# Performance work log

Hardware: AMD Instinct MI355X
Metric: run time of the kernel (lower is better)

## Reference

```python
import jax, jax.numpy as jnp
from jax import lax
import numpy as np

RATIO = 0.25
RADIUS = 0.2


def _fps(xyz, npoint):
    # iterative farthest point sampling, sequential over npoint via lax.scan
    B, N, _ = xyz.shape
    far0 = jax.random.randint(jax.random.key(42), (B,), 0, N)
    dist0 = jnp.full((B, N), 1e10, xyz.dtype)

    def step(carry, _):
        distance, far = carry
        centroid = jnp.take_along_axis(xyz, far[:, None, None], axis=1)  # (B,1,3)
        d = jnp.sum((xyz - centroid) ** 2, axis=-1)                      # (B,N)
        distance = jnp.minimum(distance, d)
        return (distance, jnp.argmax(distance, axis=-1)), far

    _, idxs = lax.scan(step, (dist0, far0), None, length=npoint)  # (npoint,B)
    return jnp.transpose(idxs)  # (B,npoint)


def _gather(pts, idx):
    # pts (B,N,C), idx (B,...) int -> (B,...,C)
    return jax.vmap(lambda p, i: p[i])(pts, idx)


def reference(xyz, points, w1, b1, w2, b2, w3, b3):
    B, N, _ = xyz.shape
    S = int(N * RATIO)
    fps_idx = _fps(xyz, S)                 # (B,S)
    new_xyz = _gather(xyz, fps_idx)        # (B,S,3)

    # ball query with nsample = N (module passes xyz.shape[1])
    sqr = (jnp.sum(new_xyz ** 2, -1)[:, :, None]
           + jnp.sum(xyz ** 2, -1)[:, None, :]
           - 2.0 * jnp.einsum('bsc,bnc->bsn', new_xyz, xyz))  # (B,S,N)
    gidx = jnp.where(sqr > RADIUS ** 2, N, jnp.arange(N)[None, None, :])
    gidx = jnp.sort(gidx, axis=-1)         # (B,S,N), sentinel N sorts last
    first = gidx[:, :, 0:1]
    idx = jnp.where(gidx == N, first, gidx)  # (B,S,N)

    grouped_xyz = _gather(xyz, idx) - new_xyz[:, :, None, :]       # (B,S,N,3)
    grouped_pts = _gather(jnp.transpose(points, (0, 2, 1)), idx)   # (B,S,N,C)
    x = jnp.concatenate([grouped_xyz, grouped_pts], axis=-1)       # (B,S,N,3+C)

    # 1x1 convs == pointwise channel linears, ReLU except last
    x = jax.nn.relu(jnp.einsum('bsnc,oc->bsno', x, w1) + b1)
    x = jax.nn.relu(jnp.einsum('bsnc,oc->bsno', x, w2) + b2)
    x = jnp.einsum('bsnc,oc->bsno', x, w3) + b3

    new_points = jnp.transpose(jnp.max(x, axis=2), (0, 2, 1))  # (B,C',S)
    return new_xyz, new_points


def setup_inputs() -> dict:
    key = jax.random.key(0)
    ks = jax.random.split(key, 8)
    return {
        'xyz': jax.random.uniform(ks[0], (2, 2048, 3), dtype=jnp.float32),
        'points': jax.random.normal(ks[1], (2, 13, 2048), dtype=jnp.float32),
        'w1': 0.1 * jax.random.normal(ks[2], (32, 16), dtype=jnp.float32),
        'b1': 0.1 * jax.random.normal(ks[3], (32,), dtype=jnp.float32),
        'w2': 0.1 * jax.random.normal(ks[4], (32, 32), dtype=jnp.float32),
        'b2': 0.1 * jax.random.normal(ks[5], (32,), dtype=jnp.float32),
        'w3': 0.1 * jax.random.normal(ks[6], (64, 32), dtype=jnp.float32),
        'b3': 0.1 * jax.random.normal(ks[7], (64,), dtype=jnp.float32),
    }
```

## Files before the change

kernel.cpp:

```cpp
#include <hip/hip_runtime.h>
#include <stdint.h>

#define NPTS 2048
#define SOUT 512
#define NB   2
#define TB   256
#define PPT  8
#define NW   4
#define FMAGIC 0xC0DE0000u

typedef float vf2 __attribute__((ext_vector_type(2)));

__device__ __forceinline__ float wave_allmax_f32(float v) {
    int x = __float_as_int(v); int t;
    t = __builtin_amdgcn_update_dpp(x, x, 0x111, 0xF, 0xF, true); v = fmaxf(v, __int_as_float(t)); x = __float_as_int(v);
    t = __builtin_amdgcn_update_dpp(x, x, 0x112, 0xF, 0xF, true); v = fmaxf(v, __int_as_float(t)); x = __float_as_int(v);
    t = __builtin_amdgcn_update_dpp(x, x, 0x114, 0xF, 0xF, true); v = fmaxf(v, __int_as_float(t)); x = __float_as_int(v);
    t = __builtin_amdgcn_update_dpp(x, x, 0x118, 0xF, 0xF, true); v = fmaxf(v, __int_as_float(t)); x = __float_as_int(v);
    t = __builtin_amdgcn_update_dpp(x, x, 0x142, 0xA, 0xF, true); v = fmaxf(v, __int_as_float(t)); x = __float_as_int(v);
    t = __builtin_amdgcn_update_dpp(x, x, 0x143, 0xC, 0xF, true); v = fmaxf(v, __int_as_float(t)); x = __float_as_int(v);
    return __int_as_float(__builtin_amdgcn_readlane(x, 63));
}
__device__ __forceinline__ float lane_bcast(float v, int l) {
    return __int_as_float(__builtin_amdgcn_readlane(__float_as_int(v), l));
}
__device__ __forceinline__ float4 sel4(bool c, float4 A, float4 B) {
    float4 r;
    r.x = c ? A.x : B.x; r.y = c ? A.y : B.y;
    r.z = c ? A.z : B.z; r.w = c ? A.w : B.w;
    return r;
}

template<bool FUSED>
__device__ __forceinline__ void fps_role(const float* __restrict__ xb,
                                         float* __restrict__ ob,
                                         unsigned* flagp, int far,
                                         float4* slot , float* scf,
                                         int t) {
    const int lane = t & 63;
    const int wvl  = t >> 6;
    float v24[24];
    {
        const float4* src = (const float4*)(xb + t * PPT * 3);
#pragma unroll
        for (int j = 0; j < 6; ++j) {
            float4 a = src[j];
            v24[j*4+0] = a.x; v24[j*4+1] = a.y; v24[j*4+2] = a.z; v24[j*4+3] = a.w;
        }
    }
    vf2 PX[4], PY[4], PZ[4], DD[4];
#pragma unroll
    for (int j = 0; j < 4; ++j) {
        PX[j].x = v24[(2*j)*3+0]; PX[j].y = v24[(2*j+1)*3+0];
        PY[j].x = v24[(2*j)*3+1]; PY[j].y = v24[(2*j+1)*3+1];
        PZ[j].x = v24[(2*j)*3+2]; PZ[j].y = v24[(2*j+1)*3+2];
        DD[j].x = 1e10f; DD[j].y = 1e10f;
    }
    float cx = xb[far*3+0], cy = xb[far*3+1], cz = xb[far*3+2];

    for (int s = 0; s < SOUT - 1; ++s) {
        if (FUSED) {
            if (wvl == 3) {
                if (lane == 32 && s >= 16 && (s & 15) == 0)
                    __hip_atomic_store(flagp, FMAGIC + (unsigned)s,
                                       __ATOMIC_RELEASE, __HIP_MEMORY_SCOPE_AGENT);
                if (lane >= 32 && lane < 35) {
                    float v = (lane == 32) ? cx : ((lane == 33) ? cy : cz);
                    unsigned* o = (unsigned*)ob + s * 3 + (lane - 32);
                    __hip_atomic_store(o, __float_as_uint(v),
                                       __ATOMIC_RELAXED, __HIP_MEMORY_SCOPE_AGENT);
                }
            }
        } else {
            if (t == 0) { scf[s*3+0] = cx; scf[s*3+1] = cy; scf[s*3+2] = cz; }
        }
        {
#pragma clang fp contract(off)
            vf2 vcx; vcx.x = cx; vcx.y = cx;
            vf2 vcy; vcy.x = cy; vcy.y = cy;
            vf2 vcz; vcz.x = cz; vcz.y = cz;
#pragma unroll
            for (int j = 0; j < 4; ++j) {
                vf2 dx = PX[j] - vcx;
                vf2 dy = PY[j] - vcy;
                vf2 dz = PZ[j] - vcz;
                vf2 d2 = (dx*dx + dy*dy) + dz*dz;
                DD[j].x = fminf(DD[j].x, d2.x);
                DD[j].y = fminf(DD[j].y, d2.y);
            }
        }
        float v1[4], x1v[4], y1v[4], z1v[4];
#pragma unroll
        for (int j = 0; j < 4; ++j) {
            bool l = DD[j].x >= DD[j].y;
            v1[j]  = l ? DD[j].x : DD[j].y;
            x1v[j] = l ? PX[j].x : PX[j].y;
            y1v[j] = l ? PY[j].x : PY[j].y;
            z1v[j] = l ? PZ[j].x : PZ[j].y;
        }
        float v2v[2], x2v[2], y2v[2], z2v[2];
#pragma unroll
        for (int j = 0; j < 2; ++j) {
            bool l = v1[2*j] >= v1[2*j+1];
            v2v[j] = l ? v1[2*j]  : v1[2*j+1];
            x2v[j] = l ? x1v[2*j] : x1v[2*j+1];
            y2v[j] = l ? y1v[2*j] : y1v[2*j+1];
            z2v[j] = l ? z1v[2*j] : z1v[2*j+1];
        }
        bool lf = v2v[0] >= v2v[1];
        float bv = lf ? v2v[0] : v2v[1];
        float bx = lf ? x2v[0] : x2v[1];
        float by = lf ? y2v[0] : y2v[1];
        float bz = lf ? z2v[0] : z2v[1];
        float wmax = wave_allmax_f32(bv);
        unsigned long long msk = __ballot(bv == wmax);
        int l0 = (int)__builtin_ctzll(msk);
        float wx = lane_bcast(bx, l0);
        float wy = lane_bcast(by, l0);
        float wz = lane_bcast(bz, l0);
        const int par = s & 1;
        if (lane == 0) slot[par*NW + wvl] = make_float4(wmax, wx, wy, wz);
        if (FUSED) {
            __builtin_amdgcn_s_waitcnt(0xC07F);
            __builtin_amdgcn_s_barrier();
        } else {
            __syncthreads();
        }
        float4 a0 = slot[par*NW + 0];
        float4 a1 = slot[par*NW + 1];
        float4 a2 = slot[par*NW + 2];
        float4 a3 = slot[par*NW + 3];
        float4 m01 = sel4(a1.x > a0.x, a1, a0);
        float4 m23 = sel4(a3.x > a2.x, a3, a2);
        float4 mf  = sel4(m23.x > m01.x, m23, m01);
        cx = mf.y; cy = mf.z; cz = mf.w;
    }
    if (FUSED) {
        if (wvl == 3) {
            if (lane >= 32 && lane < 35) {
                float v = (lane == 32) ? cx : ((lane == 33) ? cy : cz);
                unsigned* o = (unsigned*)ob + (SOUT - 1) * 3 + (lane - 32);
                __hip_atomic_store(o, __float_as_uint(v),
                                   __ATOMIC_RELAXED, __HIP_MEMORY_SCOPE_AGENT);
            }
            if (lane == 32)
                __hip_atomic_store(flagp, FMAGIC + 512u,
                                   __ATOMIC_RELEASE, __HIP_MEMORY_SCOPE_AGENT);
        }
    } else {
        if (t == 0) {
            scf[(SOUT-1)*3+0] = cx; scf[(SOUT-1)*3+1] = cy; scf[(SOUT-1)*3+2] = cz;
        }
        __syncthreads();
        for (int i = t; i < SOUT * 3; i += TB) ob[i] = scf[i];
    }
}

__device__ __forceinline__ void group_role(
        const float* __restrict__ xyz,  const float* __restrict__ points,
        const float* __restrict__ w1,   const float* __restrict__ b1,
        const float* __restrict__ w2,   const float* __restrict__ b2,
        const float* __restrict__ w3,   const float* __restrict__ b3,
        const float* __restrict__ new_xyz, float* __restrict__ new_points,
        const unsigned* flags, unsigned short* sidx, float* sh2,
        int lane, int q) {
    float wf3[32];
    {
        const float4* w3v = (const float4*)(w3 + lane * 32);
#pragma unroll
        for (int j = 0; j < 8; ++j) {
            float4 v = w3v[j];
            wf3[j*4+0] = v.x; wf3[j*4+1] = v.y; wf3[j*4+2] = v.z; wf3[j*4+3] = v.w;
        }
    }
    const float rb3 = b3[lane];
    const int b = q >> 9;
    const int s = q & (SOUT - 1);

    if (flags) {
        const unsigned* flagp = flags + (b << 6);
        if (lane == 0) {
            const unsigned tgt = FMAGIC + (unsigned)s + 1u;
            int polls = 0;
            for (;;) {
                unsigned v = __hip_atomic_load(flagp, __ATOMIC_ACQUIRE,
                                               __HIP_MEMORY_SCOPE_AGENT);
                if (v >= tgt && v <= FMAGIC + 512u) break;
                if (++polls > (1 << 18)) break;
                __builtin_amdgcn_s_sleep(32);
            }
        }
        __threadfence();
    }
    const unsigned* nx = (const unsigned*)new_xyz + (size_t)q * 3;
    const float qx = __uint_as_float(__hip_atomic_load(nx + 0, __ATOMIC_RELAXED, __HIP_MEMORY_SCOPE_AGENT));
    const float qy = __uint_as_float(__hip_atomic_load(nx + 1, __ATOMIC_RELAXED, __HIP_MEMORY_SCOPE_AGENT));
    const float qz = __uint_as_float(__hip_atomic_load(nx + 2, __ATOMIC_RELAXED, __HIP_MEMORY_SCOPE_AGENT));
    const float qs = __fadd_rn(__fadd_rn(__fmul_rn(qx,qx), __fmul_rn(qy,qy)), __fmul_rn(qz,qz));
    const float* xb = xyz    + (size_t)b * NPTS * 3;
    const float* pb = points + (size_t)b * 13 * NPTS;

    int cnt = 0;
    const unsigned long long lm = (1ull << lane) - 1ull;
    for (int r = 0; r < NPTS / 64; ++r) {
        int n = r * 64 + lane;
        float x = xb[n*3+0], y = xb[n*3+1], z = xb[n*3+2];
        float pn = __fadd_rn(__fadd_rn(__fmul_rn(x,x), __fmul_rn(y,y)), __fmul_rn(z,z));
        float dt = __fadd_rn(__fadd_rn(__fmul_rn(qx,x), __fmul_rn(qy,y)), __fmul_rn(qz,z));
        float sqr = __fsub_rn(__fadd_rn(qs, pn), __fmul_rn(2.0f, dt));
        bool sel = !(sqr > 0.04f);
        unsigned long long m = __ballot(sel);
        if (sel) sidx[cnt + __popcll(m & lm)] = (unsigned short)n;
        cnt += (int)__popcll(m);
    }
    const int K = cnt;
    const int nfirst = (int)sidx[0];

    float mx = -3.0e38f;
    for (int tb = 0; tb < K; tb += 64) {
        int m = tb + lane;
        int n = (m < K) ? (int)sidx[m] : nfirst;
        float f[16];
        f[0] = xb[n*3+0] - qx;
        f[1] = xb[n*3+1] - qy;
        f[2] = xb[n*3+2] - qz;
#pragma unroll
        for (int c = 0; c < 13; ++c) f[3+c] = pb[c*NPTS + n];
        float h1[32];
#pragma unroll
        for (int o = 0; o < 32; ++o) {
            float acc = b1[o];
            const float4* wr = (const float4*)(w1 + o*16);
#pragma unroll
            for (int c4 = 0; c4 < 4; ++c4) {
                float4 wv = wr[c4];
                acc = fmaf(f[c4*4+0], wv.x, acc);
                acc = fmaf(f[c4*4+1], wv.y, acc);
                acc = fmaf(f[c4*4+2], wv.z, acc);
                acc = fmaf(f[c4*4+3], wv.w, acc);
            }
            h1[o] = fmaxf(acc, 0.0f);
        }
        float h2[32];
#pragma unroll
        for (int o = 0; o < 32; ++o) {
            float acc = b2[o];
            const float4* wr = (const float4*)(w2 + o*32);
#pragma unroll
            for (int c4 = 0; c4 < 8; ++c4) {
                float4 wv = wr[c4];
                acc = fmaf(h1[c4*4+0], wv.x, acc);
                acc = fmaf(h1[c4*4+1], wv.y, acc);
                acc = fmaf(h1[c4*4+2], wv.z, acc);
                acc = fmaf(h1[c4*4+3], wv.w, acc);
            }
            h2[o] = fmaxf(acc, 0.0f);
        }
        {
            float4* row = (float4*)(sh2 + lane * 36);
#pragma unroll
            for (int c4 = 0; c4 < 8; ++c4)
                row[c4] = make_float4(h2[c4*4+0], h2[c4*4+1], h2[c4*4+2], h2[c4*4+3]);
        }
        int rows = K - tb; if (rows > 64) rows = 64;
#pragma unroll 4
        for (int n2 = 0; n2 < rows; ++n2) {
            const float4* hr = (const float4*)(sh2 + n2 * 36);
            float acc = rb3;
#pragma unroll
            for (int c4 = 0; c4 < 8; ++c4) {
                float4 h = hr[c4];
                acc = fmaf(h.x, wf3[c4*4+0], acc);
                acc = fmaf(h.y, wf3[c4*4+1], acc);
                acc = fmaf(h.z, wf3[c4*4+2], acc);
                acc = fmaf(h.w, wf3[c4*4+3], acc);
            }
            mx = fmaxf(mx, acc);
        }
    }
    new_points[((size_t)b * 64 + lane) * SOUT + s] = mx;
}

__global__ __launch_bounds__(TB, 1) void fused_kernel(
        const float* __restrict__ xyz,  const float* __restrict__ points,
        const float* __restrict__ w1,   const float* __restrict__ b1,
        const float* __restrict__ w2,   const float* __restrict__ b2,
        const float* __restrict__ w3,   const float* __restrict__ b3,
        float* __restrict__ new_xyz, float* __restrict__ new_points,
        unsigned* flags, int far0, int far1) {
    __shared__ float4 s_slot[2 * NW];
    __shared__ unsigned short s_sidx[4 * NPTS];
    __shared__ __align__(16) float s_sh2[4 * 64 * 36];
    const int blk = blockIdx.x;
    const int tid = threadIdx.x;
    if (blk < 2) {
        const int bg = blk;
        fps_role<true>(xyz + (size_t)bg * NPTS * 3,
                       new_xyz + (size_t)bg * SOUT * 3,
                       flags + (bg << 6),
                       (bg == 0) ? far0 : far1,
                       s_slot, nullptr, tid);
    } else {
        const int lane = tid & 63;
        const int wvl  = tid >> 6;
        const int q    = (blk - 2) * 4 + wvl;
        group_role(xyz, points, w1, b1, w2, b2, w3, b3, new_xyz, new_points,
                   flags, s_sidx + wvl * NPTS, s_sh2 + wvl * 64 * 36, lane, q);
    }
}

__global__ __launch_bounds__(TB, 1) void fps_kernel(const float* __restrict__ xyz,
                                                    float* __restrict__ new_xyz,
                                                    int far0, int far1) {
    __shared__ float4 s_slot[2 * NW];
    __shared__ __align__(16) float s_scf[SOUT * 3];
    const int bg = blockIdx.x;
    fps_role<false>(xyz + (size_t)bg * NPTS * 3, new_xyz + (size_t)bg * SOUT * 3,
                    nullptr, (bg == 0) ? far0 : far1, s_slot, s_scf, threadIdx.x);
}
__global__ __launch_bounds__(64, 1) void group_kernel(
        const float* __restrict__ xyz,  const float* __restrict__ points,
        const float* __restrict__ w1,   const float* __restrict__ b1,
        const float* __restrict__ w2,   const float* __restrict__ b2,
        const float* __restrict__ w3,   const float* __restrict__ b3,
        const float* __restrict__ new_xyz, float* __restrict__ new_points) {
    __shared__ unsigned short s_sidx[NPTS];
    __shared__ __align__(16) float s_sh2[64 * 36];
    group_role(xyz, points, w1, b1, w2, b2, w3, b3, new_xyz, new_points,
               nullptr, s_sidx, s_sh2, threadIdx.x, blockIdx.x);
}

static inline uint32_t rotl32(uint32_t x, int r) { return (x << r) | (x >> (32 - r)); }
static void threefry2x32_host(uint32_t k0, uint32_t k1, uint32_t& x0, uint32_t& x1) {
    const int R[2][4] = {{13,15,26,6},{17,29,16,24}};
    uint32_t ks[3] = {k0, k1, k0 ^ k1 ^ 0x1BD11BDAu};
    x0 += ks[0]; x1 += ks[1];
    for (int i = 0; i < 5; ++i) {
        for (int j = 0; j < 4; ++j) { x0 += x1; x1 = rotl32(x1, R[i & 1][j]); x1 ^= x0; }
        x0 += ks[(i + 1) % 3];
        x1 += ks[(i + 2) % 3] + (uint32_t)(i + 1);
    }
}

extern "C" void kernel_launch(void* const* d_in, const int* in_sizes, int n_in,
                              void* d_out, int out_size, void* d_ws, size_t ws_size,
                              hipStream_t stream) {
    const float* xyz    = (const float*)d_in[0];
    const float* points = (const float*)d_in[1];
    const float* w1 = (const float*)d_in[2];
    const float* b1 = (const float*)d_in[3];
    const float* w2 = (const float*)d_in[4];
    const float* b2 = (const float*)d_in[5];
    const float* w3 = (const float*)d_in[6];
    const float* b3 = (const float*)d_in[7];
    float* out        = (float*)d_out;
    float* new_xyz    = out;
    float* new_points = out + NB * SOUT * 3;

    uint32_t k2a = 0, k2b = 1; threefry2x32_host(0u, 42u, k2a, k2b);
    uint32_t u0 = 0, u1 = 0;  threefry2x32_host(k2a, k2b, u0, u1);
    uint32_t v0 = 0, v1 = 1;  threefry2x32_host(k2a, k2b, v0, v1);
    int far0 = (int)((u0 ^ u1) & (NPTS - 1));
    int far1 = (int)((v0 ^ v1) & (NPTS - 1));

    if (ws_size >= 512) {
        hipLaunchKernelGGL(fused_kernel, dim3(2 + NB * SOUT / 4), dim3(TB), 0, stream,
                           xyz, points, w1, b1, w2, b2, w3, b3,
                           new_xyz, new_points, (unsigned*)d_ws, far0, far1);
    } else {
        hipLaunchKernelGGL(fps_kernel, dim3(NB), dim3(TB), 0, stream,
                           xyz, new_xyz, far0, far1);
        hipLaunchKernelGGL(group_kernel, dim3(NB * SOUT), dim3(64), 0, stream,
                           xyz, points, w1, b1, w2, b2, w3, b3, new_xyz, new_points);
    }
}
```

Measured before the change: 360.9 us.

## Run farthest point sampling in a single wave to drop block barriers

The FPS role now runs on a single 64-lane wave. Each lane holds 32 points instead of 8, so the per-iteration LDS slot exchange and block barrier across four waves are gone; the wave reduction and lane broadcast alone pick the next centroid. This removes 511 serialized barriers from the sequential critical path. In exchange each wave does four times the distance work per step and uses more registers, and the other three waves of the FPS blocks sit idle.

```diff
diff --git a/kernel.cpp b/kernel.cpp
--- a/kernel.cpp
+++ b/kernel.cpp
@@ -5,8 +5,6 @@
 #define SOUT 512
 #define NB   2
 #define TB   256
-#define PPT  8
-#define NW   4
 #define FMAGIC 0xC0DE0000u
 
 typedef float vf2 __attribute__((ext_vector_type(2)));
@@ -24,135 +22,112 @@
 __device__ __forceinline__ float lane_bcast(float v, int l) {
     return __int_as_float(__builtin_amdgcn_readlane(__float_as_int(v), l));
 }
-__device__ __forceinline__ float4 sel4(bool c, float4 A, float4 B) {
-    float4 r;
-    r.x = c ? A.x : B.x; r.y = c ? A.y : B.y;
-    r.z = c ? A.z : B.z; r.w = c ? A.w : B.w;
-    return r;
-}
 
 template<bool FUSED>
-__device__ __forceinline__ void fps_role(const float* __restrict__ xb,
-                                         float* __restrict__ ob,
-                                         unsigned* flagp, int far,
-                                         float4* slot , float* scf,
-                                         int t) {
-    const int lane = t & 63;
-    const int wvl  = t >> 6;
-    float v24[24];
+__device__ __forceinline__ void fps_role_sw(const float* __restrict__ xb,
+                                            float* __restrict__ ob,
+                                            unsigned* flagp, int far, int lane) {
+    vf2 PX[16], PY[16], PZ[16], DD[16];
     {
-        const float4* src = (const float4*)(xb + t * PPT * 3);
-#pragma unroll
-        for (int j = 0; j < 6; ++j) {
-            float4 a = src[j];
-            v24[j*4+0] = a.x; v24[j*4+1] = a.y; v24[j*4+2] = a.z; v24[j*4+3] = a.w;
-        }
-    }
-    vf2 PX[4], PY[4], PZ[4], DD[4];
-#pragma unroll
-    for (int j = 0; j < 4; ++j) {
-        PX[j].x = v24[(2*j)*3+0]; PX[j].y = v24[(2*j+1)*3+0];
-        PY[j].x = v24[(2*j)*3+1]; PY[j].y = v24[(2*j+1)*3+1];
-        PZ[j].x = v24[(2*j)*3+2]; PZ[j].y = v24[(2*j+1)*3+2];
-        DD[j].x = 1e10f; DD[j].y = 1e10f;
+        const float4* src = (const float4*)(xb + (size_t)lane * 96);
+#pragma unroll
+        for (int g = 0; g < 8; ++g) {
+            float4 a  = src[g*3+0];
+            float4 b4 = src[g*3+1];
+            float4 c4 = src[g*3+2];
+            PX[2*g+0].x = a.x;  PY[2*g+0].x = a.y;  PZ[2*g+0].x = a.z;
+            PX[2*g+0].y = a.w;  PY[2*g+0].y = b4.x; PZ[2*g+0].y = b4.y;
+            PX[2*g+1].x = b4.z; PY[2*g+1].x = b4.w; PZ[2*g+1].x = c4.x;
+            PX[2*g+1].y = c4.y; PY[2*g+1].y = c4.z; PZ[2*g+1].y = c4.w;
+            DD[2*g+0].x = 1e10f; DD[2*g+0].y = 1e10f;
+            DD[2*g+1].x = 1e10f; DD[2*g+1].y = 1e10f;
+        }
     }
     float cx = xb[far*3+0], cy = xb[far*3+1], cz = xb[far*3+2];
 
     for (int s = 0; s < SOUT - 1; ++s) {
         if (FUSED) {
-            if (wvl == 3) {
-                if (lane == 32 && s >= 16 && (s & 15) == 0)
-                    __hip_atomic_store(flagp, FMAGIC + (unsigned)s,
-                                       __ATOMIC_RELEASE, __HIP_MEMORY_SCOPE_AGENT);
-                if (lane >= 32 && lane < 35) {
-                    float v = (lane == 32) ? cx : ((lane == 33) ? cy : cz);
-                    unsigned* o = (unsigned*)ob + s * 3 + (lane - 32);
-                    __hip_atomic_store(o, __float_as_uint(v),
-                                       __ATOMIC_RELAXED, __HIP_MEMORY_SCOPE_AGENT);
-                }
+            if (lane == 32 && s >= 16 && (s & 15) == 0)
+                __hip_atomic_store(flagp, FMAGIC + (unsigned)s,
+                                   __ATOMIC_RELEASE, __HIP_MEMORY_SCOPE_AGENT);
+            if (lane >= 32 && lane < 35) {
+                float v = (lane == 32) ? cx : ((lane == 33) ? cy : cz);
+                unsigned* o = (unsigned*)ob + s * 3 + (lane - 32);
+                __hip_atomic_store(o, __float_as_uint(v),
+                                   __ATOMIC_RELAXED, __HIP_MEMORY_SCOPE_AGENT);
             }
         } else {
-            if (t == 0) { scf[s*3+0] = cx; scf[s*3+1] = cy; scf[s*3+2] = cz; }
-        }
+            if (lane == 0) { ob[s*3+0] = cx; ob[s*3+1] = cy; ob[s*3+2] = cz; }
+        }
+        float bq[4], xq[4], yq[4], zq[4];
         {
 #pragma clang fp contract(off)
             vf2 vcx; vcx.x = cx; vcx.y = cx;
             vf2 vcy; vcy.x = cy; vcy.y = cy;
             vf2 vcz; vcz.x = cz; vcz.y = cz;
 #pragma unroll
-            for (int j = 0; j < 4; ++j) {
-                vf2 dx = PX[j] - vcx;
-                vf2 dy = PY[j] - vcy;
-                vf2 dz = PZ[j] - vcz;
-                vf2 d2 = (dx*dx + dy*dy) + dz*dz;
-                DD[j].x = fminf(DD[j].x, d2.x);
-                DD[j].y = fminf(DD[j].y, d2.y);
-            }
-        }
-        float v1[4], x1v[4], y1v[4], z1v[4];
-#pragma unroll
-        for (int j = 0; j < 4; ++j) {
-            bool l = DD[j].x >= DD[j].y;
-            v1[j]  = l ? DD[j].x : DD[j].y;
-            x1v[j] = l ? PX[j].x : PX[j].y;
-            y1v[j] = l ? PY[j].x : PY[j].y;
-            z1v[j] = l ? PZ[j].x : PZ[j].y;
-        }
-        float v2v[2], x2v[2], y2v[2], z2v[2];
-#pragma unroll
-        for (int j = 0; j < 2; ++j) {
-            bool l = v1[2*j] >= v1[2*j+1];
-            v2v[j] = l ? v1[2*j]  : v1[2*j+1];
-            x2v[j] = l ? x1v[2*j] : x1v[2*j+1];
-            y2v[j] = l ? y1v[2*j] : y1v[2*j+1];
-            z2v[j] = l ? z1v[2*j] : z1v[2*j+1];
-        }
-        bool lf = v2v[0] >= v2v[1];
-        float bv = lf ? v2v[0] : v2v[1];
-        float bx = lf ? x2v[0] : x2v[1];
-        float by = lf ? y2v[0] : y2v[1];
-        float bz = lf ? z2v[0] : z2v[1];
+            for (int q = 0; q < 4; ++q) {
+#pragma unroll
+                for (int jj = 0; jj < 4; ++jj) {
+                    const int j = q * 4 + jj;
+                    vf2 dx = PX[j] - vcx;
+                    vf2 dy = PY[j] - vcy;
+                    vf2 dz = PZ[j] - vcz;
+                    vf2 d2 = (dx*dx + dy*dy) + dz*dz;
+                    DD[j].x = fminf(DD[j].x, d2.x);
+                    DD[j].y = fminf(DD[j].y, d2.y);
+                    bool l  = DD[j].x >= DD[j].y;
+                    float vv = l ? DD[j].x : DD[j].y;
+                    float xx = l ? PX[j].x : PX[j].y;
+                    float yy = l ? PY[j].x : PY[j].y;
+                    float zz = l ? PZ[j].x : PZ[j].y;
+                    if (jj == 0) { bq[q] = vv; xq[q] = xx; yq[q] = yy; zq[q] = zz; }
+                    else {
+                        bool g = bq[q] >= vv;
+                        bq[q] = g ? bq[q] : vv;
+                        xq[q] = g ? xq[q] : xx;
+                        yq[q] = g ? yq[q] : yy;
+                        zq[q] = g ? zq[q] : zz;
+                    }
+                }
+            }
+        }
+        bool l01 = bq[0] >= bq[1];
+        float v01 = l01 ? bq[0] : bq[1];
+        float x01 = l01 ? xq[0] : xq[1];
+        float y01 = l01 ? yq[0] : yq[1];
+        float z01 = l01 ? zq[0] : zq[1];
+        bool l23 = bq[2] >= bq[3];
+        float v23 = l23 ? bq[2] : bq[3];
+        float x23 = l23 ? xq[2] : xq[3];
+        float y23 = l23 ? yq[2] : yq[3];
+        float z23 = l23 ? zq[2] : zq[3];
+        bool lf = v01 >= v23;
+        float bv = lf ? v01 : v23;
+        float bx = lf ? x01 : x23;
+        float by = lf ? y01 : y23;
+        float bz = lf ? z01 : z23;
         float wmax = wave_allmax_f32(bv);
         unsigned long long msk = __ballot(bv == wmax);
         int l0 = (int)__builtin_ctzll(msk);
-        float wx = lane_bcast(bx, l0);
-        float wy = lane_bcast(by, l0);
-        float wz = lane_bcast(bz, l0);
-        const int par = s & 1;
-        if (lane == 0) slot[par*NW + wvl] = make_float4(wmax, wx, wy, wz);
-        if (FUSED) {
-            __builtin_amdgcn_s_waitcnt(0xC07F);
-            __builtin_amdgcn_s_barrier();
-        } else {
-            __syncthreads();
-        }
-        float4 a0 = slot[par*NW + 0];
-        float4 a1 = slot[par*NW + 1];
-        float4 a2 = slot[par*NW + 2];
-        float4 a3 = slot[par*NW + 3];
-        float4 m01 = sel4(a1.x > a0.x, a1, a0);
-        float4 m23 = sel4(a3.x > a2.x, a3, a2);
-        float4 mf  = sel4(m23.x > m01.x, m23, m01);
-        cx = mf.y; cy = mf.z; cz = mf.w;
+        cx = lane_bcast(bx, l0);
+        cy = lane_bcast(by, l0);
+        cz = lane_bcast(bz, l0);
     }
     if (FUSED) {
-        if (wvl == 3) {
-            if (lane >= 32 && lane < 35) {
-                float v = (lane == 32) ? cx : ((lane == 33) ? cy : cz);
-                unsigned* o = (unsigned*)ob + (SOUT - 1) * 3 + (lane - 32);
-                __hip_atomic_store(o, __float_as_uint(v),
-                                   __ATOMIC_RELAXED, __HIP_MEMORY_SCOPE_AGENT);
-            }
-            if (lane == 32)
-                __hip_atomic_store(flagp, FMAGIC + 512u,
-                                   __ATOMIC_RELEASE, __HIP_MEMORY_SCOPE_AGENT);
-        }
+        if (lane >= 32 && lane < 35) {
+            float v = (lane == 32) ? cx : ((lane == 33) ? cy : cz);
+            unsigned* o = (unsigned*)ob + (SOUT - 1) * 3 + (lane - 32);
+            __hip_atomic_store(o, __float_as_uint(v),
+                               __ATOMIC_RELAXED, __HIP_MEMORY_SCOPE_AGENT);
+        }
+        if (lane == 32)
+            __hip_atomic_store(flagp, FMAGIC + 512u,
+                               __ATOMIC_RELEASE, __HIP_MEMORY_SCOPE_AGENT);
     } else {
-        if (t == 0) {
-            scf[(SOUT-1)*3+0] = cx; scf[(SOUT-1)*3+1] = cy; scf[(SOUT-1)*3+2] = cz;
-        }
-        __syncthreads();
-        for (int i = t; i < SOUT * 3; i += TB) ob[i] = scf[i];
+        if (lane == 0) {
+            ob[(SOUT-1)*3+0] = cx; ob[(SOUT-1)*3+1] = cy; ob[(SOUT-1)*3+2] = cz;
+        }
     }
 }
 
@@ -288,35 +263,34 @@
         const float* __restrict__ w3,   const float* __restrict__ b3,
         float* __restrict__ new_xyz, float* __restrict__ new_points,
         unsigned* flags, int far0, int far1) {
-    __shared__ float4 s_slot[2 * NW];
     __shared__ unsigned short s_sidx[4 * NPTS];
     __shared__ __align__(16) float s_sh2[4 * 64 * 36];
     const int blk = blockIdx.x;
     const int tid = threadIdx.x;
     if (blk < 2) {
-        const int bg = blk;
-        fps_role<true>(xyz + (size_t)bg * NPTS * 3,
-                       new_xyz + (size_t)bg * SOUT * 3,
-                       flags + (bg << 6),
-                       (bg == 0) ? far0 : far1,
-                       s_slot, nullptr, tid);
-    } else {
-        const int lane = tid & 63;
-        const int wvl  = tid >> 6;
-        const int q    = (blk - 2) * 4 + wvl;
-        group_role(xyz, points, w1, b1, w2, b2, w3, b3, new_xyz, new_points,
-                   flags, s_sidx + wvl * NPTS, s_sh2 + wvl * 64 * 36, lane, q);
-    }
+        if (tid < 64) {
+            fps_role_sw<true>(xyz + (size_t)blk * NPTS * 3,
+                              new_xyz + (size_t)blk * SOUT * 3,
+                              flags + (blk << 6),
+                              (blk == 0) ? far0 : far1, tid);
+        }
+        return;
+    }
+    const int lane = tid & 63;
+    const int wvl  = tid >> 6;
+    const int q    = (blk - 2) * 4 + wvl;
+    group_role(xyz, points, w1, b1, w2, b2, w3, b3, new_xyz, new_points,
+               flags, s_sidx + wvl * NPTS, s_sh2 + wvl * 64 * 36, lane, q);
 }
 
 __global__ __launch_bounds__(TB, 1) void fps_kernel(const float* __restrict__ xyz,
                                                     float* __restrict__ new_xyz,
                                                     int far0, int far1) {
-    __shared__ float4 s_slot[2 * NW];
-    __shared__ __align__(16) float s_scf[SOUT * 3];
     const int bg = blockIdx.x;
-    fps_role<false>(xyz + (size_t)bg * NPTS * 3, new_xyz + (size_t)bg * SOUT * 3,
-                    nullptr, (bg == 0) ? far0 : far1, s_slot, s_scf, threadIdx.x);
+    if (threadIdx.x < 64)
+        fps_role_sw<false>(xyz + (size_t)bg * NPTS * 3,
+                           new_xyz + (size_t)bg * SOUT * 3,
+                           nullptr, (bg == 0) ? far0 : far1, threadIdx.x);
 }
 __global__ __launch_bounds__(64, 1) void group_kernel(
         const float* __restrict__ xyz,  const float* __restrict__ points,
```

Result: slower. 533.3 us (+47.8%).

## Spread FPS over 8 waves and give each group wave two queries

Applied to the files above, without the earlier changes.

The FPS block grows from 256 to 512 threads (8 waves, 4 points per thread), which shortens the per-thread distance update and local argmax chain on the sequential critical path. The winning lane now writes its slot directly, dropping three readlane broadcasts, and the cross-wave reduction covers 8 slots. The fused grid shrinks: each group block runs 4 active waves of its 8, and each wave handles two query indices (widx and widx+512). This trades a longer per-wave group workload and idle waves for less sequential work per FPS iteration.

```diff
diff --git a/kernel.cpp b/kernel.cpp
--- a/kernel.cpp
+++ b/kernel.cpp
@@ -4,9 +4,10 @@
 #define NPTS 2048
 #define SOUT 512
 #define NB   2
-#define TB   256
-#define PPT  8
-#define NW   4
+#define TB   512
+#define NW   8
+#define PPT  4
+#define GW   4
 #define FMAGIC 0xC0DE0000u
 
 typedef float vf2 __attribute__((ext_vector_type(2)));
@@ -21,9 +22,6 @@
     t = __builtin_amdgcn_update_dpp(x, x, 0x143, 0xC, 0xF, true); v = fmaxf(v, __int_as_float(t)); x = __float_as_int(v);
     return __int_as_float(__builtin_amdgcn_readlane(x, 63));
 }
-__device__ __forceinline__ float lane_bcast(float v, int l) {
-    return __int_as_float(__builtin_amdgcn_readlane(__float_as_int(v), l));
-}
 __device__ __forceinline__ float4 sel4(bool c, float4 A, float4 B) {
     float4 r;
     r.x = c ? A.x : B.x; r.y = c ? A.y : B.y;
@@ -32,35 +30,31 @@
 }
 
 template<bool FUSED>
-__device__ __forceinline__ void fps_role(const float* __restrict__ xb,
-                                         float* __restrict__ ob,
-                                         unsigned* flagp, int far,
-                                         float4* slot , float* scf,
-                                         int t) {
+__device__ __forceinline__ void fps_role8(const float* __restrict__ xb,
+                                          float* __restrict__ ob,
+                                          unsigned* flagp, int far,
+                                          float4* slot , float* scf,
+                                          int t) {
     const int lane = t & 63;
     const int wvl  = t >> 6;
-    float v24[24];
+    vf2 PX[2], PY[2], PZ[2], DD[2];
     {
-        const float4* src = (const float4*)(xb + t * PPT * 3);
-#pragma unroll
-        for (int j = 0; j < 6; ++j) {
-            float4 a = src[j];
-            v24[j*4+0] = a.x; v24[j*4+1] = a.y; v24[j*4+2] = a.z; v24[j*4+3] = a.w;
-        }
-    }
-    vf2 PX[4], PY[4], PZ[4], DD[4];
-#pragma unroll
-    for (int j = 0; j < 4; ++j) {
-        PX[j].x = v24[(2*j)*3+0]; PX[j].y = v24[(2*j+1)*3+0];
-        PY[j].x = v24[(2*j)*3+1]; PY[j].y = v24[(2*j+1)*3+1];
-        PZ[j].x = v24[(2*j)*3+2]; PZ[j].y = v24[(2*j+1)*3+2];
-        DD[j].x = 1e10f; DD[j].y = 1e10f;
+        const float4* src = (const float4*)(xb + (size_t)t * (PPT * 3));
+        float4 a  = src[0];
+        float4 b4 = src[1];
+        float4 c4 = src[2];
+        PX[0].x = a.x;  PY[0].x = a.y;  PZ[0].x = a.z;
+        PX[0].y = a.w;  PY[0].y = b4.x; PZ[0].y = b4.y;
+        PX[1].x = b4.z; PY[1].x = b4.w; PZ[1].x = c4.x;
+        PX[1].y = c4.y; PY[1].y = c4.z; PZ[1].y = c4.w;
+        DD[0].x = 1e10f; DD[0].y = 1e10f;
+        DD[1].x = 1e10f; DD[1].y = 1e10f;
     }
     float cx = xb[far*3+0], cy = xb[far*3+1], cz = xb[far*3+2];
 
     for (int s = 0; s < SOUT - 1; ++s) {
         if (FUSED) {
-            if (wvl == 3) {
+            if (wvl == NW - 1) {
                 if (lane == 32 && s >= 16 && (s & 15) == 0)
                     __hip_atomic_store(flagp, FMAGIC + (unsigned)s,
                                        __ATOMIC_RELEASE, __HIP_MEMORY_SCOPE_AGENT);
@@ -80,7 +74,7 @@
             vf2 vcy; vcy.x = cy; vcy.y = cy;
             vf2 vcz; vcz.x = cz; vcz.y = cz;
 #pragma unroll
-            for (int j = 0; j < 4; ++j) {
+            for (int j = 0; j < 2; ++j) {
                 vf2 dx = PX[j] - vcx;
                 vf2 dy = PY[j] - vcy;
                 vf2 dz = PZ[j] - vcz;
@@ -89,37 +83,26 @@
                 DD[j].y = fminf(DD[j].y, d2.y);
             }
         }
-        float v1[4], x1v[4], y1v[4], z1v[4];
-#pragma unroll
-        for (int j = 0; j < 4; ++j) {
-            bool l = DD[j].x >= DD[j].y;
-            v1[j]  = l ? DD[j].x : DD[j].y;
-            x1v[j] = l ? PX[j].x : PX[j].y;
-            y1v[j] = l ? PY[j].x : PY[j].y;
-            z1v[j] = l ? PZ[j].x : PZ[j].y;
-        }
-        float v2v[2], x2v[2], y2v[2], z2v[2];
-#pragma unroll
-        for (int j = 0; j < 2; ++j) {
-            bool l = v1[2*j] >= v1[2*j+1];
-            v2v[j] = l ? v1[2*j]  : v1[2*j+1];
-            x2v[j] = l ? x1v[2*j] : x1v[2*j+1];
-            y2v[j] = l ? y1v[2*j] : y1v[2*j+1];
-            z2v[j] = l ? z1v[2*j] : z1v[2*j+1];
-        }
-        bool lf = v2v[0] >= v2v[1];
-        float bv = lf ? v2v[0] : v2v[1];
-        float bx = lf ? x2v[0] : x2v[1];
-        float by = lf ? y2v[0] : y2v[1];
-        float bz = lf ? z2v[0] : z2v[1];
+        bool la = DD[0].x >= DD[0].y;
+        float va = la ? DD[0].x : DD[0].y;
+        float ax = la ? PX[0].x : PX[0].y;
+        float ay = la ? PY[0].x : PY[0].y;
+        float az = la ? PZ[0].x : PZ[0].y;
+        bool lb = DD[1].x >= DD[1].y;
+        float vb = lb ? DD[1].x : DD[1].y;
+        float ex = lb ? PX[1].x : PX[1].y;
+        float ey = lb ? PY[1].x : PY[1].y;
+        float ez = lb ? PZ[1].x : PZ[1].y;
+        bool gm = va >= vb;
+        float bv = gm ? va : vb;
+        float bx = gm ? ax : ex;
+        float by = gm ? ay : ey;
+        float bz = gm ? az : ez;
         float wmax = wave_allmax_f32(bv);
         unsigned long long msk = __ballot(bv == wmax);
         int l0 = (int)__builtin_ctzll(msk);
-        float wx = lane_bcast(bx, l0);
-        float wy = lane_bcast(by, l0);
-        float wz = lane_bcast(bz, l0);
         const int par = s & 1;
-        if (lane == 0) slot[par*NW + wvl] = make_float4(wmax, wx, wy, wz);
+        if (lane == l0) slot[par*NW + wvl] = make_float4(wmax, bx, by, bz);
         if (FUSED) {
             __builtin_amdgcn_s_waitcnt(0xC07F);
             __builtin_amdgcn_s_barrier();
@@ -130,13 +113,21 @@
         float4 a1 = slot[par*NW + 1];
         float4 a2 = slot[par*NW + 2];
         float4 a3 = slot[par*NW + 3];
+        float4 a4 = slot[par*NW + 4];
+        float4 a5 = slot[par*NW + 5];
+        float4 a6 = slot[par*NW + 6];
+        float4 a7 = slot[par*NW + 7];
         float4 m01 = sel4(a1.x > a0.x, a1, a0);
         float4 m23 = sel4(a3.x > a2.x, a3, a2);
-        float4 mf  = sel4(m23.x > m01.x, m23, m01);
+        float4 m45 = sel4(a5.x > a4.x, a5, a4);
+        float4 m67 = sel4(a7.x > a6.x, a7, a6);
+        float4 mA  = sel4(m23.x > m01.x, m23, m01);
+        float4 mB  = sel4(m67.x > m45.x, m67, m45);
+        float4 mf  = sel4(mB.x > mA.x, mB, mA);
         cx = mf.y; cy = mf.z; cz = mf.w;
     }
     if (FUSED) {
-        if (wvl == 3) {
+        if (wvl == NW - 1) {
             if (lane >= 32 && lane < 35) {
                 float v = (lane == 32) ? cx : ((lane == 33) ? cy : cz);
                 unsigned* o = (unsigned*)ob + (SOUT - 1) * 3 + (lane - 32);
@@ -289,24 +280,28 @@
         float* __restrict__ new_xyz, float* __restrict__ new_points,
         unsigned* flags, int far0, int far1) {
     __shared__ float4 s_slot[2 * NW];
-    __shared__ unsigned short s_sidx[4 * NPTS];
-    __shared__ __align__(16) float s_sh2[4 * 64 * 36];
+    __shared__ unsigned short s_sidx[GW * NPTS];
+    __shared__ __align__(16) float s_sh2[GW * 64 * 36];
     const int blk = blockIdx.x;
     const int tid = threadIdx.x;
     if (blk < 2) {
-        const int bg = blk;
-        fps_role<true>(xyz + (size_t)bg * NPTS * 3,
-                       new_xyz + (size_t)bg * SOUT * 3,
-                       flags + (bg << 6),
-                       (bg == 0) ? far0 : far1,
-                       s_slot, nullptr, tid);
-    } else {
-        const int lane = tid & 63;
-        const int wvl  = tid >> 6;
-        const int q    = (blk - 2) * 4 + wvl;
-        group_role(xyz, points, w1, b1, w2, b2, w3, b3, new_xyz, new_points,
-                   flags, s_sidx + wvl * NPTS, s_sh2 + wvl * 64 * 36, lane, q);
-    }
+        fps_role8<true>(xyz + (size_t)blk * NPTS * 3,
+                        new_xyz + (size_t)blk * SOUT * 3,
+                        flags + (blk << 6),
+                        (blk == 0) ? far0 : far1,
+                        s_slot, nullptr, tid);
+        return;
+    }
+    const int lane = tid & 63;
+    const int wvl  = tid >> 6;
+    if (wvl >= GW) return;
+    const int widx = (blk - 2) * GW + wvl;
+    unsigned short* sx = s_sidx + wvl * NPTS;
+    float* sh = s_sh2 + (size_t)wvl * 64 * 36;
+    group_role(xyz, points, w1, b1, w2, b2, w3, b3, new_xyz, new_points,
+               flags, sx, sh, lane, widx);
+    group_role(xyz, points, w1, b1, w2, b2, w3, b3, new_xyz, new_points,
+               flags, sx, sh, lane, widx + 512);
 }
 
 __global__ __launch_bounds__(TB, 1) void fps_kernel(const float* __restrict__ xyz,
@@ -315,8 +310,8 @@
     __shared__ float4 s_slot[2 * NW];
     __shared__ __align__(16) float s_scf[SOUT * 3];
     const int bg = blockIdx.x;
-    fps_role<false>(xyz + (size_t)bg * NPTS * 3, new_xyz + (size_t)bg * SOUT * 3,
-                    nullptr, (bg == 0) ? far0 : far1, s_slot, s_scf, threadIdx.x);
+    fps_role8<false>(xyz + (size_t)bg * NPTS * 3, new_xyz + (size_t)bg * SOUT * 3,
+                     nullptr, (bg == 0) ? far0 : far1, s_slot, s_scf, threadIdx.x);
 }
 __global__ __launch_bounds__(64, 1) void group_kernel(
         const float* __restrict__ xyz,  const float* __restrict__ points,
@@ -364,7 +359,7 @@
     int far1 = (int)((v0 ^ v1) & (NPTS - 1));
 
     if (ws_size >= 512) {
-        hipLaunchKernelGGL(fused_kernel, dim3(2 + NB * SOUT / 4), dim3(TB), 0, stream,
+        hipLaunchKernelGGL(fused_kernel, dim3(2 + NB * SOUT / (2 * GW)), dim3(TB), 0, stream,
                            xyz, points, w1, b1, w2, b2, w3, b3,
                            new_xyz, new_points, (unsigned*)d_ws, far0, far1);
     } else {
```

Result: slower. 460.8 us (+27.7%).
